# Kernel tuning notes

Measured on AMD Instinct MI355X. Metric: run time of the kernel, lower is better.

Reference implementation:

```python
import jax, jax.numpy as jnp
import numpy as np

DIM = 4096
N_HEADS = 32
N_KV_HEADS = 8
HEAD_DIM = DIM // N_HEADS  # 128
KV_DIM = N_KV_HEADS * HEAD_DIM  # 1024
B, T = 2, 1024


def setup_inputs() -> dict:
    key = jax.random.key(0)
    ks = jax.random.split(key, 5)
    s1 = 1.0 / np.sqrt(DIM)
    return {
        "x": jax.random.normal(ks[0], (B, T, DIM), dtype=jnp.float32),
        "W1": jax.random.uniform(ks[1], (DIM + 2 * KV_DIM, DIM), dtype=jnp.float32, minval=-s1, maxval=s1),
        "b1": jax.random.uniform(ks[2], (DIM + 2 * KV_DIM,), dtype=jnp.float32, minval=-s1, maxval=s1),
        "W2": jax.random.uniform(ks[3], (DIM, DIM), dtype=jnp.float32, minval=-s1, maxval=s1),
        "b2": jax.random.uniform(ks[4], (DIM,), dtype=jnp.float32, minval=-s1, maxval=s1),
    }


def reference(x, W1, b1, W2, b2):
    Bn, Tn, D = x.shape
    G = N_HEADS // N_KV_HEADS
    qkv = x @ W1.T + b1  # [B,T,D+2*KV_DIM]
    q = qkv[:, :, :DIM]
    k = qkv[:, :, DIM:DIM + KV_DIM]
    v = qkv[:, :, DIM + KV_DIM:]
    # Faithful to torch repeat_interleave(G, dim=-1): scalar-level interleave on flat feature dim
    k = jnp.repeat(k, G, axis=-1)  # [B,T,D]
    v = jnp.repeat(v, G, axis=-1)
    q = q.reshape(Bn, Tn, N_HEADS, HEAD_DIM).transpose(0, 2, 1, 3)  # [B,H,T,hd]
    k = k.reshape(Bn, Tn, N_HEADS, HEAD_DIM).transpose(0, 2, 1, 3)
    v = v.reshape(Bn, Tn, N_HEADS, HEAD_DIM).transpose(0, 2, 1, 3)
    scale = 1.0 / jnp.sqrt(jnp.asarray(HEAD_DIM, dtype=x.dtype))
    qk = jnp.einsum('bhqd,bhkd->bhqk', q, k) * scale  # [B,H,T,T]
    causal = jnp.tril(jnp.ones((Tn, Tn), dtype=bool))
    qk = jnp.where(causal[None, None], qk, jnp.asarray(-jnp.inf, dtype=qk.dtype))
    att = jax.nn.softmax(qk, axis=-1)
    out = jnp.einsum('bhqk,bhkd->bhqd', att, v)  # [B,H,T,hd]
    out = out.transpose(0, 2, 1, 3).reshape(Bn, Tn, D)
    return out @ W2.T + b2
```

## Files before the change

kernel.cpp:

```cpp
#include <hip/hip_runtime.h>

#define DIMX  4096
#define NH    32
#define HD    128
#define BB    2
#define TT    1024
#define MROWS (BB*TT)
#define CQKV  3072
#define SCALE_Q 0.12751743f

typedef _Float16 half_t;
typedef __attribute__((ext_vector_type(4))) _Float16 f16x4;
typedef __attribute__((ext_vector_type(8))) _Float16 f16x8;
typedef __attribute__((ext_vector_type(4))) float    f32x4;

__device__ __forceinline__ void async_copy16(const void* gsrc, void* ldst) {
  __builtin_amdgcn_global_load_lds(
      (const __attribute__((address_space(1))) unsigned int*)gsrc,
      (__attribute__((address_space(3))) unsigned int*)ldst,
      16, 0, 0);
}

__global__ __launch_bounds__(256) void cvt_f32_f16_kernel(
    const float4* __restrict__ src, f16x4* __restrict__ dst, int n4) {
  int stride = gridDim.x * blockDim.x;
  for (int i = blockIdx.x * blockDim.x + threadIdx.x; i < n4; i += stride) {
    float4 f = src[i];
    f16x4 h;
    h.x = (_Float16)f.x; h.y = (_Float16)f.y;
    h.z = (_Float16)f.z; h.w = (_Float16)f.w;
    dst[i] = h;
  }
}

__global__ __launch_bounds__(256) void fold_w1_kernel(
    const float* __restrict__ W1, const float* __restrict__ b1,
    half_t* __restrict__ W1f, float* __restrict__ b1f)
{
  long idx = (long)blockIdx.x * 256 + threadIdx.x;
  int row = (int)(idx >> 10);
  int c4  = ((int)idx & 1023) << 2;
  f16x4 h;
  if (row < 1024) {
    const float* s = W1 + ((long)row << 2) * DIMX + c4;
    float4 a = *(const float4*)s;
    float4 b = *(const float4*)(s + DIMX);
    float4 c = *(const float4*)(s + 2 * DIMX);
    float4 d = *(const float4*)(s + 3 * DIMX);
    h.x = (_Float16)((a.x + b.x + c.x + d.x) * SCALE_Q);
    h.y = (_Float16)((a.y + b.y + c.y + d.y) * SCALE_Q);
    h.z = (_Float16)((a.z + b.z + c.z + d.z) * SCALE_Q);
    h.w = (_Float16)((a.w + b.w + c.w + d.w) * SCALE_Q);
    if (c4 == 0) {
      const float* bb = b1 + ((long)row << 2);
      b1f[row] = (bb[0] + bb[1] + bb[2] + bb[3]) * SCALE_Q;
    }
  } else {
    const float* s = W1 + ((long)(row + 3072)) * DIMX + c4;
    float4 a = *(const float4*)s;
    h.x = (_Float16)a.x; h.y = (_Float16)a.y;
    h.z = (_Float16)a.z; h.w = (_Float16)a.w;
    if (c4 == 0) b1f[row] = b1[row + 3072];
  }
  *(f16x4*)&W1f[(long)row * DIMX + c4] = h;
}

__global__ __launch_bounds__(256) void fold_w2_kernel(
    const float* __restrict__ W2, half_t* __restrict__ W2f)
{
  long idx = (long)blockIdx.x * 256 + threadIdx.x;
  int row = (int)(idx >> 8);
  int j4  = ((int)idx & 255) << 2;
  const float* s = W2 + (long)row * DIMX + ((long)j4 << 2);
  float4 a = *(const float4*)s;
  float4 b = *(const float4*)(s + 4);
  float4 c = *(const float4*)(s + 8);
  float4 d = *(const float4*)(s + 12);
  f16x4 h;
  h.x = (_Float16)(a.x + a.y + a.z + a.w);
  h.y = (_Float16)(b.x + b.y + b.z + b.w);
  h.z = (_Float16)(c.x + c.y + c.z + c.w);
  h.w = (_Float16)(d.x + d.y + d.z + d.w);
  *(f16x4*)&W2f[(long)row * 1024 + j4] = h;
}

template<int OUT_IS_F16>
__global__ __launch_bounds__(256) void gemm_nt_bias(
    const half_t* __restrict__ A, const half_t* __restrict__ Bw,
    const float* __restrict__ bias, void* __restrict__ Cout,
    int M, int N, int K)
{
  __shared__ alignas(16) half_t As[128 * 32];
  __shared__ alignas(16) half_t Bs[128 * 32];

  const int tid  = threadIdx.x;
  const int lane = tid & 63;
  const int w    = tid >> 6;
  const long row0 = (long)blockIdx.y * 128;
  const long col0 = (long)blockIdx.x * 128;

  const int rr = tid >> 2;
  const int cc = (tid & 3) * 8;
  const half_t* ga0 = A  + (row0 + rr)      * K + cc;
  const half_t* ga1 = A  + (row0 + 64 + rr) * K + cc;
  const half_t* gb0 = Bw + (col0 + rr)      * K + cc;
  const half_t* gb1 = Bw + (col0 + 64 + rr) * K + cc;
  half_t* la0 = &As[w * 512];
  half_t* la1 = &As[2048 + w * 512];
  half_t* lb0 = &Bs[w * 512];
  half_t* lb1 = &Bs[2048 + w * 512];

  const int wm = (w >> 1) * 64;
  const int wn = (w & 1) * 64;
  const int fr = lane & 15;
  const int fk = (lane >> 4) * 8;
  const half_t* pa = &As[(wm + fr) * 32 + fk];
  const half_t* pb = &Bs[(wn + fr) * 32 + fk];

  f32x4 acc[4][4] = {};

  for (int kt = 0; kt < K; kt += 32) {
    __syncthreads();
    async_copy16(ga0 + kt, la0);
    async_copy16(ga1 + kt, la1);
    async_copy16(gb0 + kt, lb0);
    async_copy16(gb1 + kt, lb1);
    __syncthreads();

    f16x8 af[4], bf[4];
#pragma unroll
    for (int mi = 0; mi < 4; ++mi) af[mi] = *(const f16x8*)(pa + mi * 16 * 32);
#pragma unroll
    for (int ni = 0; ni < 4; ++ni) bf[ni] = *(const f16x8*)(pb + ni * 16 * 32);
#pragma unroll
    for (int mi = 0; mi < 4; ++mi)
#pragma unroll
      for (int ni = 0; ni < 4; ++ni)
        acc[mi][ni] = __builtin_amdgcn_mfma_f32_16x16x32_f16(
            af[mi], bf[ni], acc[mi][ni], 0, 0, 0);
  }

  const int er = (lane >> 4) * 4;
  const int ec = lane & 15;
#pragma unroll
  for (int mi = 0; mi < 4; ++mi) {
#pragma unroll
    for (int ni = 0; ni < 4; ++ni) {
      long gn = col0 + wn + ni * 16 + ec;
      float bv = bias[gn];
#pragma unroll
      for (int r = 0; r < 4; ++r) {
        long gm = row0 + wm + mi * 16 + er + r;
        float v = acc[mi][ni][r] + bv;
        if (OUT_IS_F16) ((half_t*)Cout)[gm * N + gn] = (half_t)v;
        else            ((float*)Cout)[gm * N + gn]  = v;
      }
    }
  }
}

__global__ __launch_bounds__(256) void gemm_nt_splitk(
    const half_t* __restrict__ A, const half_t* __restrict__ Bw,
    float* __restrict__ Cp0, float* __restrict__ Cp1,
    int M, int N, int K)
{
  __shared__ alignas(16) half_t As[128 * 32];
  __shared__ alignas(16) half_t Bs[128 * 32];

  const int tid  = threadIdx.x;
  const int lane = tid & 63;
  const int w    = tid >> 6;
  const long row0 = (long)blockIdx.y * 128;
  const long col0 = (long)blockIdx.x * 128;
  const int  KH   = K >> 1;
  const long k0   = (long)blockIdx.z * KH;

  const int rr = tid >> 2;
  const int cc = (tid & 3) * 8;
  const half_t* ga0 = A  + (row0 + rr)      * K + k0 + cc;
  const half_t* ga1 = A  + (row0 + 64 + rr) * K + k0 + cc;
  const half_t* gb0 = Bw + (col0 + rr)      * K + k0 + cc;
  const half_t* gb1 = Bw + (col0 + 64 + rr) * K + k0 + cc;
  half_t* la0 = &As[w * 512];
  half_t* la1 = &As[2048 + w * 512];
  half_t* lb0 = &Bs[w * 512];
  half_t* lb1 = &Bs[2048 + w * 512];

  const int wm = (w >> 1) * 64;
  const int wn = (w & 1) * 64;
  const int fr = lane & 15;
  const int fk = (lane >> 4) * 8;
  const half_t* pa = &As[(wm + fr) * 32 + fk];
  const half_t* pb = &Bs[(wn + fr) * 32 + fk];

  f32x4 acc[4][4] = {};

  for (int kt = 0; kt < KH; kt += 32) {
    __syncthreads();
    async_copy16(ga0 + kt, la0);
    async_copy16(ga1 + kt, la1);
    async_copy16(gb0 + kt, lb0);
    async_copy16(gb1 + kt, lb1);
    __syncthreads();

    f16x8 af[4], bf[4];
#pragma unroll
    for (int mi = 0; mi < 4; ++mi) af[mi] = *(const f16x8*)(pa + mi * 16 * 32);
#pragma unroll
    for (int ni = 0; ni < 4; ++ni) bf[ni] = *(const f16x8*)(pb + ni * 16 * 32);
#pragma unroll
    for (int mi = 0; mi < 4; ++mi)
#pragma unroll
      for (int ni = 0; ni < 4; ++ni)
        acc[mi][ni] = __builtin_amdgcn_mfma_f32_16x16x32_f16(
            af[mi], bf[ni], acc[mi][ni], 0, 0, 0);
  }

  float* Cp = blockIdx.z ? Cp1 : Cp0;
  const int er = (lane >> 4) * 4;
  const int ec = lane & 15;
#pragma unroll
  for (int mi = 0; mi < 4; ++mi) {
#pragma unroll
    for (int ni = 0; ni < 4; ++ni) {
      long gn = col0 + wn + ni * 16 + ec;
#pragma unroll
      for (int r = 0; r < 4; ++r) {
        long gm = row0 + wm + mi * 16 + er + r;
        Cp[gm * N + gn] = acc[mi][ni][r];
      }
    }
  }
}

__global__ __launch_bounds__(256) void splitk_reduce_kernel(
    const float4* __restrict__ C0, const float4* __restrict__ C1,
    const float4* __restrict__ bias4, f16x4* __restrict__ dst)
{
  const int col  = blockIdx.x * 256 + threadIdx.x;
  const long row = blockIdx.y;
  const long i   = row * (CQKV / 4) + col;
  float4 a = C0[i];
  float4 b = C1[i];
  float4 bv = bias4[col];
  f16x4 h;
  h.x = (_Float16)(a.x + b.x + bv.x);
  h.y = (_Float16)(a.y + b.y + bv.y);
  h.z = (_Float16)(a.z + b.z + bv.z);
  h.w = (_Float16)(a.w + b.w + bv.w);
  dst[i] = h;
}

#define VTS 72
#define PSS 72
__global__ __launch_bounds__(256, 4) void attn_kernel(
    const half_t* __restrict__ qkv,
    half_t* __restrict__ attc)
{
  __shared__ alignas(16) half_t Ks[64 * 32];
  __shared__ alignas(16) half_t Vt[48 * VTS];
  __shared__ alignas(16) half_t Ps[4][16 * PSS];

  const int tid  = threadIdx.x;
  const int lane = tid & 63;
  const int w    = tid >> 6;
  const int low  = lane & 15;
  const int quad = lane >> 4;
  const int bh   = blockIdx.y;
  const int b    = bh >> 5;
  const int h    = bh & 31;
  const long rb  = (long)b * TT;

  if (tid < 8) {
    f16x8 one;
#pragma unroll
    for (int i = 0; i < 8; ++i) one[i] = (_Float16)1.0f;
    *(f16x8*)&Vt[32 * VTS + tid * 8] = one;
  }

  const int srow = tid >> 2;
  const int sc4  = (tid & 3) << 3;
  half_t* ksdst  = &Ks[w * 512];
  half_t* psw    = &Ps[w][0];
  float*  Ob     = (float*)psw;

  for (int pass = 0; pass < 2; ++pass) {
    const int tile = pass ? (int)blockIdx.x : 15 - (int)blockIdx.x;
    const int t0   = tile * 64;
    const int qg   = t0 + 16 * w;

    f16x8 qf = *(const f16x8*)&qkv[(rb + qg + low) * CQKV + h * 32 + quad * 8];

    f32x4 acc0 = {}, acc1 = {}, acc2 = {};
    const f32x4 zero = {};

    for (int c = 0; c <= t0; c += 64) {
      __syncthreads();
      const half_t* kg = &qkv[(rb + c + srow) * CQKV + 1024 + h * 32 + sc4];
      async_copy16(kg, ksdst);
      f16x8 vv = *(const f16x8*)(kg + 1024);
#pragma unroll
      for (int j = 0; j < 8; ++j)
        Vt[(sc4 + j) * VTS + srow] = vv[j];
      __syncthreads();

      f32x4 s[4];
#pragma unroll
      for (int st = 0; st < 4; ++st) {
        f16x8 kf = *(const f16x8*)&Ks[(st * 16 + low) * 32 + quad * 8];
        s[st] = __builtin_amdgcn_mfma_f32_16x16x32_f16(qf, kf, zero, 0, 0, 0);
      }

      const bool diag = (c == t0);
#pragma unroll
      for (int st = 0; st < 4; ++st) {
#pragma unroll
        for (int r = 0; r < 4; ++r) {
          const int key = c + st * 16 + low;
          const int q   = qg + 4 * quad + r;
          float p = __builtin_amdgcn_exp2f(s[st][r]);
          if (diag && key > q) p = 0.f;
          psw[(4 * quad + r) * PSS + st * 16 + low] = (_Float16)p;
        }
      }

      f16x8 p0 = *(const f16x8*)&psw[low * PSS + 0 * 32 + quad * 8];
      f16x8 p1 = *(const f16x8*)&psw[low * PSS + 1 * 32 + quad * 8];

      f16x8 v00 = *(const f16x8*)&Vt[(0  + low) * VTS + 0  + quad * 8];
      f16x8 v01 = *(const f16x8*)&Vt[(0  + low) * VTS + 32 + quad * 8];
      f16x8 v10 = *(const f16x8*)&Vt[(16 + low) * VTS + 0  + quad * 8];
      f16x8 v11 = *(const f16x8*)&Vt[(16 + low) * VTS + 32 + quad * 8];
      f16x8 v20 = *(const f16x8*)&Vt[(32 + low) * VTS + 0  + quad * 8];
      f16x8 v21 = *(const f16x8*)&Vt[(32 + low) * VTS + 32 + quad * 8];

      acc0 = __builtin_amdgcn_mfma_f32_16x16x32_f16(v00, p0, acc0, 0, 0, 0);
      acc0 = __builtin_amdgcn_mfma_f32_16x16x32_f16(v01, p1, acc0, 0, 0, 0);
      acc1 = __builtin_amdgcn_mfma_f32_16x16x32_f16(v10, p0, acc1, 0, 0, 0);
      acc1 = __builtin_amdgcn_mfma_f32_16x16x32_f16(v11, p1, acc1, 0, 0, 0);
      acc2 = __builtin_amdgcn_mfma_f32_16x16x32_f16(v20, p0, acc2, 0, 0, 0);
      acc2 = __builtin_amdgcn_mfma_f32_16x16x32_f16(v21, p1, acc2, 0, 0, 0);
    }

    __syncthreads();

    float linv = 1.0f / __shfl(acc2[0], low);

#pragma unroll
    for (int r = 0; r < 4; ++r) {
      Ob[low * 36 + 0  + 4 * quad + r] = acc0[r] * linv;
      Ob[low * 36 + 16 + 4 * quad + r] = acc1[r] * linv;
    }
    __syncthreads();

    f16x8 ov;
#pragma unroll
    for (int i = 0; i < 8; ++i)
      ov[i] = (_Float16)Ob[low * 36 + quad * 8 + i];
    *(f16x8*)&attc[(rb + qg + low) * 1024 + h * 32 + quad * 8] = ov;
  }
}

extern "C" void kernel_launch(void* const* d_in, const int* in_sizes, int n_in,
                              void* d_out, int out_size, void* d_ws, size_t ws_size,
                              hipStream_t stream) {
  (void)in_sizes; (void)n_in; (void)out_size; (void)ws_size;
  const float* x  = (const float*)d_in[0];
  const float* W1 = (const float*)d_in[1];
  const float* b1 = (const float*)d_in[2];
  const float* W2 = (const float*)d_in[3];
  const float* b2 = (const float*)d_in[4];
  float* out = (float*)d_out;

  const size_t nX   = (size_t)MROWS * DIMX;
  const size_t nW1f = (size_t)CQKV  * DIMX;
  const size_t nW2f = (size_t)DIMX  * 1024;
  const size_t nQKV = (size_t)MROWS * CQKV;
  const size_t nATT = (size_t)MROWS * 1024;

  half_t* ws   = (half_t*)d_ws;
  half_t* xh   = ws;
  half_t* w1f  = xh   + nX;
  half_t* w2f  = w1f  + nW1f;
  half_t* qkvc = w2f  + nW2f;
  half_t* attc = qkvc + nQKV;
  float*  b1f  = (float*)(attc + nATT);
  float*  c1   = (float*)(b1f + 4096);

  cvt_f32_f16_kernel<<<4096, 256, 0, stream>>>((const float4*)x, (f16x4*)xh,
                                               (int)(nX / 4));
  fold_w1_kernel<<<12288, 256, 0, stream>>>(W1, b1, w1f, b1f);
  fold_w2_kernel<<<4096, 256, 0, stream>>>(W2, w2f);

  gemm_nt_splitk<<<dim3(CQKV / 128, MROWS / 128, 2), 256, 0, stream>>>(
      xh, w1f, out , c1 , MROWS, CQKV, DIMX);
  splitk_reduce_kernel<<<dim3(CQKV / 4 / 256, MROWS), 256, 0, stream>>>(
      (const float4*)out, (const float4*)c1, (const float4*)b1f,
      (f16x4*)qkvc);

  attn_kernel<<<dim3(8, BB * NH), 256, 0, stream>>>(qkvc, attc);

  gemm_nt_bias<0><<<dim3(DIMX / 128, MROWS / 128), 256, 0, stream>>>(
      attc, w2f, b2, (void*)out, MROWS, DIMX, 1024);
}
```

Baseline: 367.8 us.

## Widen GEMM K-tile to 64 with XOR-swizzled LDS; one query tile per attention block

```diff
diff --git a/kernel.cpp b/kernel.cpp
--- a/kernel.cpp
+++ b/kernel.cpp
@@ -84,88 +84,14 @@
   *(f16x4*)&W2f[(long)row * 1024 + j4] = h;
 }
 
-template<int OUT_IS_F16>
-__global__ __launch_bounds__(256) void gemm_nt_bias(
-    const half_t* __restrict__ A, const half_t* __restrict__ Bw,
-    const float* __restrict__ bias, void* __restrict__ Cout,
-    int M, int N, int K)
-{
-  __shared__ alignas(16) half_t As[128 * 32];
-  __shared__ alignas(16) half_t Bs[128 * 32];
-
-  const int tid  = threadIdx.x;
-  const int lane = tid & 63;
-  const int w    = tid >> 6;
-  const long row0 = (long)blockIdx.y * 128;
-  const long col0 = (long)blockIdx.x * 128;
-
-  const int rr = tid >> 2;
-  const int cc = (tid & 3) * 8;
-  const half_t* ga0 = A  + (row0 + rr)      * K + cc;
-  const half_t* ga1 = A  + (row0 + 64 + rr) * K + cc;
-  const half_t* gb0 = Bw + (col0 + rr)      * K + cc;
-  const half_t* gb1 = Bw + (col0 + 64 + rr) * K + cc;
-  half_t* la0 = &As[w * 512];
-  half_t* la1 = &As[2048 + w * 512];
-  half_t* lb0 = &Bs[w * 512];
-  half_t* lb1 = &Bs[2048 + w * 512];
-
-  const int wm = (w >> 1) * 64;
-  const int wn = (w & 1) * 64;
-  const int fr = lane & 15;
-  const int fk = (lane >> 4) * 8;
-  const half_t* pa = &As[(wm + fr) * 32 + fk];
-  const half_t* pb = &Bs[(wn + fr) * 32 + fk];
-
-  f32x4 acc[4][4] = {};
-
-  for (int kt = 0; kt < K; kt += 32) {
-    __syncthreads();
-    async_copy16(ga0 + kt, la0);
-    async_copy16(ga1 + kt, la1);
-    async_copy16(gb0 + kt, lb0);
-    async_copy16(gb1 + kt, lb1);
-    __syncthreads();
-
-    f16x8 af[4], bf[4];
-#pragma unroll
-    for (int mi = 0; mi < 4; ++mi) af[mi] = *(const f16x8*)(pa + mi * 16 * 32);
-#pragma unroll
-    for (int ni = 0; ni < 4; ++ni) bf[ni] = *(const f16x8*)(pb + ni * 16 * 32);
-#pragma unroll
-    for (int mi = 0; mi < 4; ++mi)
-#pragma unroll
-      for (int ni = 0; ni < 4; ++ni)
-        acc[mi][ni] = __builtin_amdgcn_mfma_f32_16x16x32_f16(
-            af[mi], bf[ni], acc[mi][ni], 0, 0, 0);
-  }
-
-  const int er = (lane >> 4) * 4;
-  const int ec = lane & 15;
-#pragma unroll
-  for (int mi = 0; mi < 4; ++mi) {
-#pragma unroll
-    for (int ni = 0; ni < 4; ++ni) {
-      long gn = col0 + wn + ni * 16 + ec;
-      float bv = bias[gn];
-#pragma unroll
-      for (int r = 0; r < 4; ++r) {
-        long gm = row0 + wm + mi * 16 + er + r;
-        float v = acc[mi][ni][r] + bv;
-        if (OUT_IS_F16) ((half_t*)Cout)[gm * N + gn] = (half_t)v;
-        else            ((float*)Cout)[gm * N + gn]  = v;
-      }
-    }
-  }
-}
-
-__global__ __launch_bounds__(256) void gemm_nt_splitk(
+
+__global__ __launch_bounds__(256, 3) void gemm_nt_splitk(
     const half_t* __restrict__ A, const half_t* __restrict__ Bw,
     float* __restrict__ Cp0, float* __restrict__ Cp1,
     int M, int N, int K)
 {
-  __shared__ alignas(16) half_t As[128 * 32];
-  __shared__ alignas(16) half_t Bs[128 * 32];
+  __shared__ alignas(16) half_t As[128 * 64];
+  __shared__ alignas(16) half_t Bs[128 * 64];
 
   const int tid  = threadIdx.x;
   const int lane = tid & 63;
@@ -175,45 +101,59 @@
   const int  KH   = K >> 1;
   const long k0   = (long)blockIdx.z * KH;
 
-  const int rr = tid >> 2;
-  const int cc = (tid & 3) * 8;
-  const half_t* ga0 = A  + (row0 + rr)      * K + k0 + cc;
-  const half_t* ga1 = A  + (row0 + 64 + rr) * K + k0 + cc;
-  const half_t* gb0 = Bw + (col0 + rr)      * K + k0 + cc;
-  const half_t* gb1 = Bw + (col0 + 64 + rr) * K + k0 + cc;
-  half_t* la0 = &As[w * 512];
-  half_t* la1 = &As[2048 + w * 512];
-  half_t* lb0 = &Bs[w * 512];
-  half_t* lb1 = &Bs[2048 + w * 512];
+  const int rr = tid >> 3;
+  const int cs = (((tid & 7) ^ (rr & 7)) << 3);
+  const half_t* ga[4]; const half_t* gb[4];
+#pragma unroll
+  for (int i = 0; i < 4; ++i) {
+    ga[i] = A  + (row0 + i * 32 + rr) * K + k0 + cs;
+    gb[i] = Bw + (col0 + i * 32 + rr) * K + k0 + cs;
+  }
+  half_t* lds_a = &As[w * 512];
+  half_t* lds_b = &Bs[w * 512];
 
   const int wm = (w >> 1) * 64;
   const int wn = (w & 1) * 64;
-  const int fr = lane & 15;
-  const int fk = (lane >> 4) * 8;
-  const half_t* pa = &As[(wm + fr) * 32 + fk];
-  const half_t* pb = &Bs[(wn + fr) * 32 + fk];
+  const int fr   = lane & 15;
+  const int quad = lane >> 4;
+  const int rsw  = fr & 7;
+  const int o0 = ((quad ^ rsw) << 3);
+  const int o1 = (((quad | 4) ^ rsw) << 3);
+  const half_t* paw = &As[(wm + fr) * 64];
+  const half_t* pbw = &Bs[(wn + fr) * 64];
 
   f32x4 acc[4][4] = {};
 
-  for (int kt = 0; kt < KH; kt += 32) {
-    __syncthreads();
-    async_copy16(ga0 + kt, la0);
-    async_copy16(ga1 + kt, la1);
-    async_copy16(gb0 + kt, lb0);
-    async_copy16(gb1 + kt, lb1);
+  for (int kt = 0; kt < KH; kt += 64) {
+    __syncthreads();
+#pragma unroll
+    for (int i = 0; i < 4; ++i) async_copy16(ga[i] + kt, lds_a + i * 2048);
+#pragma unroll
+    for (int i = 0; i < 4; ++i) async_copy16(gb[i] + kt, lds_b + i * 2048);
     __syncthreads();
 
     f16x8 af[4], bf[4];
 #pragma unroll
-    for (int mi = 0; mi < 4; ++mi) af[mi] = *(const f16x8*)(pa + mi * 16 * 32);
-#pragma unroll
-    for (int ni = 0; ni < 4; ++ni) bf[ni] = *(const f16x8*)(pb + ni * 16 * 32);
+    for (int mi = 0; mi < 4; ++mi) af[mi] = *(const f16x8*)(paw + mi * 1024 + o0);
+#pragma unroll
+    for (int ni = 0; ni < 4; ++ni) bf[ni] = *(const f16x8*)(pbw + ni * 1024 + o0);
 #pragma unroll
     for (int mi = 0; mi < 4; ++mi)
 #pragma unroll
       for (int ni = 0; ni < 4; ++ni)
         acc[mi][ni] = __builtin_amdgcn_mfma_f32_16x16x32_f16(
             af[mi], bf[ni], acc[mi][ni], 0, 0, 0);
+
+#pragma unroll
+    for (int mi = 0; mi < 4; ++mi) af[mi] = *(const f16x8*)(paw + mi * 1024 + o1);
+#pragma unroll
+    for (int ni = 0; ni < 4; ++ni) bf[ni] = *(const f16x8*)(pbw + ni * 1024 + o1);
+#pragma unroll
+    for (int mi = 0; mi < 4; ++mi)
+#pragma unroll
+      for (int ni = 0; ni < 4; ++ni)
+        acc[mi][ni] = __builtin_amdgcn_mfma_f32_16x16x32_f16(
+            af[mi], bf[ni], acc[mi][ni], 0, 0, 0);
   }
 
   float* Cp = blockIdx.z ? Cp1 : Cp0;
@@ -228,6 +168,95 @@
       for (int r = 0; r < 4; ++r) {
         long gm = row0 + wm + mi * 16 + er + r;
         Cp[gm * N + gn] = acc[mi][ni][r];
+      }
+    }
+  }
+}
+
+template<int OUT_IS_F16>
+__global__ __launch_bounds__(256, 3) void gemm_nt_bias(
+    const half_t* __restrict__ A, const half_t* __restrict__ Bw,
+    const float* __restrict__ bias, void* __restrict__ Cout,
+    int M, int N, int K)
+{
+  __shared__ alignas(16) half_t As[128 * 64];
+  __shared__ alignas(16) half_t Bs[128 * 64];
+
+  const int tid  = threadIdx.x;
+  const int lane = tid & 63;
+  const int w    = tid >> 6;
+  const long row0 = (long)blockIdx.y * 128;
+  const long col0 = (long)blockIdx.x * 128;
+
+  const int rr = tid >> 3;
+  const int cs = (((tid & 7) ^ (rr & 7)) << 3);
+  const half_t* ga[4]; const half_t* gb[4];
+#pragma unroll
+  for (int i = 0; i < 4; ++i) {
+    ga[i] = A  + (row0 + i * 32 + rr) * K + cs;
+    gb[i] = Bw + (col0 + i * 32 + rr) * K + cs;
+  }
+  half_t* lds_a = &As[w * 512];
+  half_t* lds_b = &Bs[w * 512];
+
+  const int wm = (w >> 1) * 64;
+  const int wn = (w & 1) * 64;
+  const int fr   = lane & 15;
+  const int quad = lane >> 4;
+  const int rsw  = fr & 7;
+  const int o0 = ((quad ^ rsw) << 3);
+  const int o1 = (((quad | 4) ^ rsw) << 3);
+  const half_t* paw = &As[(wm + fr) * 64];
+  const half_t* pbw = &Bs[(wn + fr) * 64];
+
+  f32x4 acc[4][4] = {};
+
+  for (int kt = 0; kt < K; kt += 64) {
+    __syncthreads();
+#pragma unroll
+    for (int i = 0; i < 4; ++i) async_copy16(ga[i] + kt, lds_a + i * 2048);
+#pragma unroll
+    for (int i = 0; i < 4; ++i) async_copy16(gb[i] + kt, lds_b + i * 2048);
+    __syncthreads();
+
+    f16x8 af[4], bf[4];
+#pragma unroll
+    for (int mi = 0; mi < 4; ++mi) af[mi] = *(const f16x8*)(paw + mi * 1024 + o0);
+#pragma unroll
+    for (int ni = 0; ni < 4; ++ni) bf[ni] = *(const f16x8*)(pbw + ni * 1024 + o0);
+#pragma unroll
+    for (int mi = 0; mi < 4; ++mi)
+#pragma unroll
+      for (int ni = 0; ni < 4; ++ni)
+        acc[mi][ni] = __builtin_amdgcn_mfma_f32_16x16x32_f16(
+            af[mi], bf[ni], acc[mi][ni], 0, 0, 0);
+
+#pragma unroll
+    for (int mi = 0; mi < 4; ++mi) af[mi] = *(const f16x8*)(paw + mi * 1024 + o1);
+#pragma unroll
+    for (int ni = 0; ni < 4; ++ni) bf[ni] = *(const f16x8*)(pbw + ni * 1024 + o1);
+#pragma unroll
+    for (int mi = 0; mi < 4; ++mi)
+#pragma unroll
+      for (int ni = 0; ni < 4; ++ni)
+        acc[mi][ni] = __builtin_amdgcn_mfma_f32_16x16x32_f16(
+            af[mi], bf[ni], acc[mi][ni], 0, 0, 0);
+  }
+
+  const int er = (lane >> 4) * 4;
+  const int ec = lane & 15;
+#pragma unroll
+  for (int mi = 0; mi < 4; ++mi) {
+#pragma unroll
+    for (int ni = 0; ni < 4; ++ni) {
+      long gn = col0 + wn + ni * 16 + ec;
+      float bv = bias[gn];
+#pragma unroll
+      for (int r = 0; r < 4; ++r) {
+        long gm = row0 + wm + mi * 16 + er + r;
+        float v = acc[mi][ni][r] + bv;
+        if (OUT_IS_F16) ((half_t*)Cout)[gm * N + gn] = (half_t)v;
+        else            ((float*)Cout)[gm * N + gn]  = v;
       }
     }
   }
@@ -284,81 +313,79 @@
   half_t* psw    = &Ps[w][0];
   float*  Ob     = (float*)psw;
 
-  for (int pass = 0; pass < 2; ++pass) {
-    const int tile = pass ? (int)blockIdx.x : 15 - (int)blockIdx.x;
-    const int t0   = tile * 64;
-    const int qg   = t0 + 16 * w;
-
-    f16x8 qf = *(const f16x8*)&qkv[(rb + qg + low) * CQKV + h * 32 + quad * 8];
-
-    f32x4 acc0 = {}, acc1 = {}, acc2 = {};
-    const f32x4 zero = {};
-
-    for (int c = 0; c <= t0; c += 64) {
-      __syncthreads();
-      const half_t* kg = &qkv[(rb + c + srow) * CQKV + 1024 + h * 32 + sc4];
-      async_copy16(kg, ksdst);
-      f16x8 vv = *(const f16x8*)(kg + 1024);
-#pragma unroll
-      for (int j = 0; j < 8; ++j)
-        Vt[(sc4 + j) * VTS + srow] = vv[j];
-      __syncthreads();
-
-      f32x4 s[4];
-#pragma unroll
-      for (int st = 0; st < 4; ++st) {
-        f16x8 kf = *(const f16x8*)&Ks[(st * 16 + low) * 32 + quad * 8];
-        s[st] = __builtin_amdgcn_mfma_f32_16x16x32_f16(qf, kf, zero, 0, 0, 0);
+  const int tile = blockIdx.x;
+  const int t0   = tile * 64;
+  const int qg   = t0 + 16 * w;
+
+  f16x8 qf = *(const f16x8*)&qkv[(rb + qg + low) * CQKV + h * 32 + quad * 8];
+
+  f32x4 acc0 = {}, acc1 = {}, acc2 = {};
+  const f32x4 zero = {};
+
+  for (int c = 0; c <= t0; c += 64) {
+    __syncthreads();
+    const half_t* kg = &qkv[(rb + c + srow) * CQKV + 1024 + h * 32 + sc4];
+    async_copy16(kg, ksdst);
+    f16x8 vv = *(const f16x8*)(kg + 1024);
+#pragma unroll
+    for (int j = 0; j < 8; ++j)
+      Vt[(sc4 + j) * VTS + srow] = vv[j];
+    __syncthreads();
+
+    f32x4 s[4];
+#pragma unroll
+    for (int st = 0; st < 4; ++st) {
+      f16x8 kf = *(const f16x8*)&Ks[(st * 16 + low) * 32 + quad * 8];
+      s[st] = __builtin_amdgcn_mfma_f32_16x16x32_f16(qf, kf, zero, 0, 0, 0);
+    }
+
+    const bool diag = (c == t0);
+#pragma unroll
+    for (int st = 0; st < 4; ++st) {
+#pragma unroll
+      for (int r = 0; r < 4; ++r) {
+        const int key = c + st * 16 + low;
+        const int q   = qg + 4 * quad + r;
+        float p = __builtin_amdgcn_exp2f(s[st][r]);
+        if (diag && key > q) p = 0.f;
+        psw[(4 * quad + r) * PSS + st * 16 + low] = (_Float16)p;
       }
-
-      const bool diag = (c == t0);
-#pragma unroll
-      for (int st = 0; st < 4; ++st) {
-#pragma unroll
-        for (int r = 0; r < 4; ++r) {
-          const int key = c + st * 16 + low;
-          const int q   = qg + 4 * quad + r;
-          float p = __builtin_amdgcn_exp2f(s[st][r]);
-          if (diag && key > q) p = 0.f;
-          psw[(4 * quad + r) * PSS + st * 16 + low] = (_Float16)p;
-        }
-      }
-
-      f16x8 p0 = *(const f16x8*)&psw[low * PSS + 0 * 32 + quad * 8];
-      f16x8 p1 = *(const f16x8*)&psw[low * PSS + 1 * 32 + quad * 8];
-
-      f16x8 v00 = *(const f16x8*)&Vt[(0  + low) * VTS + 0  + quad * 8];
-      f16x8 v01 = *(const f16x8*)&Vt[(0  + low) * VTS + 32 + quad * 8];
-      f16x8 v10 = *(const f16x8*)&Vt[(16 + low) * VTS + 0  + quad * 8];
-      f16x8 v11 = *(const f16x8*)&Vt[(16 + low) * VTS + 32 + quad * 8];
-      f16x8 v20 = *(const f16x8*)&Vt[(32 + low) * VTS + 0  + quad * 8];
-      f16x8 v21 = *(const f16x8*)&Vt[(32 + low) * VTS + 32 + quad * 8];
-
-      acc0 = __builtin_amdgcn_mfma_f32_16x16x32_f16(v00, p0, acc0, 0, 0, 0);
-      acc0 = __builtin_amdgcn_mfma_f32_16x16x32_f16(v01, p1, acc0, 0, 0, 0);
-      acc1 = __builtin_amdgcn_mfma_f32_16x16x32_f16(v10, p0, acc1, 0, 0, 0);
-      acc1 = __builtin_amdgcn_mfma_f32_16x16x32_f16(v11, p1, acc1, 0, 0, 0);
-      acc2 = __builtin_amdgcn_mfma_f32_16x16x32_f16(v20, p0, acc2, 0, 0, 0);
-      acc2 = __builtin_amdgcn_mfma_f32_16x16x32_f16(v21, p1, acc2, 0, 0, 0);
     }
 
-    __syncthreads();
-
-    float linv = 1.0f / __shfl(acc2[0], low);
-
-#pragma unroll
-    for (int r = 0; r < 4; ++r) {
-      Ob[low * 36 + 0  + 4 * quad + r] = acc0[r] * linv;
-      Ob[low * 36 + 16 + 4 * quad + r] = acc1[r] * linv;
-    }
-    __syncthreads();
-
-    f16x8 ov;
-#pragma unroll
-    for (int i = 0; i < 8; ++i)
-      ov[i] = (_Float16)Ob[low * 36 + quad * 8 + i];
-    *(f16x8*)&attc[(rb + qg + low) * 1024 + h * 32 + quad * 8] = ov;
-  }
+    f16x8 p0 = *(const f16x8*)&psw[low * PSS + 0 * 32 + quad * 8];
+    f16x8 p1 = *(const f16x8*)&psw[low * PSS + 1 * 32 + quad * 8];
+
+    f16x8 v00 = *(const f16x8*)&Vt[(0  + low) * VTS + 0  + quad * 8];
+    f16x8 v01 = *(const f16x8*)&Vt[(0  + low) * VTS + 32 + quad * 8];
+    f16x8 v10 = *(const f16x8*)&Vt[(16 + low) * VTS + 0  + quad * 8];
+    f16x8 v11 = *(const f16x8*)&Vt[(16 + low) * VTS + 32 + quad * 8];
+    f16x8 v20 = *(const f16x8*)&Vt[(32 + low) * VTS + 0  + quad * 8];
+    f16x8 v21 = *(const f16x8*)&Vt[(32 + low) * VTS + 32 + quad * 8];
+
+    acc0 = __builtin_amdgcn_mfma_f32_16x16x32_f16(v00, p0, acc0, 0, 0, 0);
+    acc0 = __builtin_amdgcn_mfma_f32_16x16x32_f16(v01, p1, acc0, 0, 0, 0);
+    acc1 = __builtin_amdgcn_mfma_f32_16x16x32_f16(v10, p0, acc1, 0, 0, 0);
+    acc1 = __builtin_amdgcn_mfma_f32_16x16x32_f16(v11, p1, acc1, 0, 0, 0);
+    acc2 = __builtin_amdgcn_mfma_f32_16x16x32_f16(v20, p0, acc2, 0, 0, 0);
+    acc2 = __builtin_amdgcn_mfma_f32_16x16x32_f16(v21, p1, acc2, 0, 0, 0);
+  }
+
+  __syncthreads();
+
+  float linv = 1.0f / __shfl(acc2[0], low);
+
+#pragma unroll
+  for (int r = 0; r < 4; ++r) {
+    Ob[low * 36 + 0  + 4 * quad + r] = acc0[r] * linv;
+    Ob[low * 36 + 16 + 4 * quad + r] = acc1[r] * linv;
+  }
+  __syncthreads();
+
+  f16x8 ov;
+#pragma unroll
+  for (int i = 0; i < 8; ++i)
+    ov[i] = (_Float16)Ob[low * 36 + quad * 8 + i];
+  *(f16x8*)&attc[(rb + qg + low) * 1024 + h * 32 + quad * 8] = ov;
 }
 
 extern "C" void kernel_launch(void* const* d_in, const int* in_sizes, int n_in,
@@ -398,7 +425,7 @@
       (const float4*)out, (const float4*)c1, (const float4*)b1f,
       (f16x4*)qkvc);
 
-  attn_kernel<<<dim3(8, BB * NH), 256, 0, stream>>>(qkvc, attc);
+  attn_kernel<<<dim3(16, BB * NH), 256, 0, stream>>>(qkvc, attc);
 
   gemm_nt_bias<0><<<dim3(DIMX / 128, MROWS / 128), 256, 0, stream>>>(
       attc, w2f, b2, (void*)out, MROWS, DIMX, 1024);
```

New measurement: 344.0 us. 1.07x faster.
